# Kernel tuning notes

Measured on AMD Instinct MI355X. Metric: run time of the kernel, lower is better.

Reference implementation:

```python
import jax, jax.numpy as jnp
import numpy as np

B, IN, H, OUT = 4096, 1024, 2048, 1024
EPS = 1e-5  # added to std (not variance), matching the torch module


def _ln(z, a, b):
    # torch.std default is unbiased (ddof=1); eps added to sigma
    mu = jnp.mean(z, axis=1, keepdims=True)
    sigma = jnp.std(z, axis=1, ddof=1, keepdims=True)
    return (z - mu) / (sigma + EPS) * a + b


def setup_inputs() -> dict:
    key = jax.random.key(0)
    ks = iter(jax.random.split(key, 40))
    W = lambda i, o: (jax.random.normal(next(ks), (o, i), jnp.float32) / np.sqrt(i)).astype(jnp.float32)
    bz = lambda o: jnp.zeros((o,), jnp.float32)
    d = {
        "inp": jax.random.normal(next(ks), (B, IN), jnp.float32),
        "h_0": jax.random.normal(next(ks), (B, H), jnp.float32),
        "c_0": jax.random.normal(next(ks), (B, H), jnp.float32),
        # h-side gate linears (H -> H)
        "Wfh": W(H, H), "bfh": bz(H), "Wih": W(H, H), "bih": bz(H),
        "Wch": W(H, H), "bch": bz(H), "Woh": W(H, H), "boh": bz(H),
        # x-side gate linears (IN -> H)
        "Wfx": W(IN, H), "bfx": bz(H), "Wix": W(IN, H), "bix": bz(H),
        "Wcx": W(IN, H), "bcx": bz(H), "Wox": W(IN, H), "box": bz(H),
        # decoder (H -> OUT)
        "Wdec": W(H, OUT), "bdec": bz(OUT),
        # LayerNormalization params (a2 ones, b2 zeros), shape (1, H)
        "ax": jnp.ones((1, H), jnp.float32), "bx": jnp.zeros((1, H), jnp.float32),
        "ah": jnp.ones((1, H), jnp.float32), "bh": jnp.zeros((1, H), jnp.float32),
        "ac": jnp.ones((1, H), jnp.float32), "bc": jnp.zeros((1, H), jnp.float32),
    }
    return d


def reference(inp, h_0, c_0,
              Wfh, bfh, Wih, bih, Wch, bch, Woh, boh,
              Wfx, bfx, Wix, bix, Wcx, bcx, Wox, box,
              Wdec, bdec, ax, bx, ah, bh, ac, bc):
    lin = lambda x, W, b: x @ W.T + b
    gate = lambda wx, bx_, wh, bh_: (_ln(lin(inp, wx, bx_), ax, bx)
                                     + _ln(lin(h_0, wh, bh_), ah, bh))
    f_g = jax.nn.sigmoid(gate(Wfx, bfx, Wfh, bfh))
    i_g = jax.nn.sigmoid(gate(Wix, bix, Wih, bih))
    c_tilda = jnp.tanh(gate(Wcx, bcx, Wch, bch))
    cx = f_g * c_0 + i_g * c_tilda
    o_g = jax.nn.sigmoid(gate(Wox, box, Woh, boh))
    hx = o_g * jnp.tanh(_ln(cx, ac, bc))
    out = lin(hx, Wdec, bdec)  # decoder applied to hidden state (vectorized over batch)
    return (out, hx, cx)
```

## Files before the change

### kernel.cpp

```cpp
#include <hip/hip_runtime.h>

#define NB   4096
#define NIN  1024
#define NH   2048
#define NOUT 1024
#define NH4  8192

typedef short short8 __attribute__((ext_vector_type(8)));
typedef float f32x4 __attribute__((ext_vector_type(4)));
typedef unsigned short ushort8v __attribute__((ext_vector_type(8)));

__device__ __forceinline__ float bf2f(unsigned short u) {
  union { unsigned int i; float f; } c; c.i = ((unsigned int)u) << 16; return c.f;
}
__device__ __forceinline__ unsigned short f2bf(float f) {
  union { float f; unsigned int i; } c; c.f = f;
  unsigned int u = c.i;
  u += 0x7FFFu + ((u >> 16) & 1u);
  return (unsigned short)(u >> 16);
}
__device__ __forceinline__ float sigf(float x) { return 1.0f / (1.0f + __expf(-x)); }
__device__ __forceinline__ float tanh_f(float x) { return 1.0f - 2.0f / (__expf(2.0f * x) + 1.0f); }

#define CNT_INP  ((size_t)NB * NIN)
#define CNT_H0   ((size_t)NB * NH)
#define CNT_WXG  ((size_t)NH * NIN)
#define CNT_WHG  ((size_t)NH * NH)
#define CNT_WD   ((size_t)NOUT * NH)
#define OFF_XB   ((size_t)0)
#define OFF_H0B  (OFF_XB + CNT_INP)
#define OFF_HXB  (OFF_H0B + CNT_H0)
#define OFF_WX   (OFF_HXB + CNT_H0)
#define OFF_WH   (OFF_WX + 4 * CNT_WXG)
#define OFF_WD   (OFF_WH + 4 * CNT_WHG)
#define OFF_ZX   (OFF_WD + CNT_WD)
#define OFF_ZH   (OFF_ZX + (size_t)NB * NH4)
#define CVT_TOTAL (OFF_WD + CNT_WD)

struct CvtArgs { const float* src[11]; };

__global__ __launch_bounds__(256) void cvt_all(CvtArgs a, unsigned short* __restrict__ dstBase) {
  const size_t i = ((size_t)blockIdx.x * 256 + threadIdx.x) * 8;
  if (i >= CVT_TOTAL) return;
  const size_t cnt[11] = {CNT_INP, CNT_H0, CNT_WXG, CNT_WXG, CNT_WXG, CNT_WXG,
                          CNT_WHG, CNT_WHG, CNT_WHG, CNT_WHG, CNT_WD};
  const size_t dst[11] = {OFF_XB, OFF_H0B,
                          OFF_WX, OFF_WX + CNT_WXG, OFF_WX + 2 * CNT_WXG, OFF_WX + 3 * CNT_WXG,
                          OFF_WH, OFF_WH + CNT_WHG, OFF_WH + 2 * CNT_WHG, OFF_WH + 3 * CNT_WHG,
                          OFF_WD};
  size_t base = 0;
#pragma unroll
  for (int s = 0; s < 11; s++) {
    if (i < base + cnt[s]) {
      const size_t off = i - base;
      const float* sp = a.src[s] + off;
      float4 v0 = *(const float4*)(sp);
      float4 v1 = *(const float4*)(sp + 4);
      ushort8v o;
      o[0] = f2bf(v0.x); o[1] = f2bf(v0.y); o[2] = f2bf(v0.z); o[3] = f2bf(v0.w);
      o[4] = f2bf(v1.x); o[5] = f2bf(v1.y); o[6] = f2bf(v1.z); o[7] = f2bf(v1.w);
      *(ushort8v*)(dstBase + dst[s] + off) = o;
      return;
    }
    base += cnt[s];
  }
}

__device__ __forceinline__ void gload16(const void* g, void* l) {
  __builtin_amdgcn_global_load_lds((const __attribute__((address_space(1))) void*)g,
                                   (__attribute__((address_space(3))) void*)l, 16, 0, 0);
}

template<int MF, bool BOUT>
__device__ __forceinline__ void gemm_core(const unsigned short* __restrict__ A,
                                          const unsigned short* __restrict__ Bm,
                                          const float* b0p, const float* b1p,
                                          const float* b2p, const float* b3p,
                                          float* __restrict__ Cf, unsigned short* __restrict__ Cb,
                                          int N, int K) {
  constexpr int TM = MF * 32;
  __shared__ __align__(16) unsigned short As[TM * 32];
  __shared__ __align__(16) unsigned short Bs[128 * 32];
  const int t = threadIdx.x;
  const int w = t >> 6;
  const int lane = t & 63;
  const int m0 = blockIdx.y * TM;
  const int n0 = blockIdx.x * 128;
  const int wm = (w >> 1) * (MF * 16);
  const int wn = (w & 1) * 64;

  f32x4 acc[MF][4];
#pragma unroll
  for (int i = 0; i < MF; i++)
#pragma unroll
    for (int j = 0; j < 4; j++) { f32x4 z = {0.f, 0.f, 0.f, 0.f}; acc[i][j] = z; }

  const int srow = t >> 2;
  const int scb = (t & 3) ^ ((srow >> 1) & 3);
  const unsigned short* Ag = A + (size_t)(m0 + srow) * K + scb * 8;
  const unsigned short* Bg = Bm + (size_t)(n0 + srow) * K + scb * 8;
  const size_t rowStep = (size_t)64 * K;
  unsigned short* AsW0 = As + w * 512;
  unsigned short* AsW1 = (MF == 4) ? (As + 2048 + w * 512) : (As + w * 512);
  unsigned short* BsW0 = Bs + w * 512;
  unsigned short* BsW1 = Bs + 2048 + w * 512;

  const int fr = lane & 15;
  const int fks = (((lane >> 4) ^ ((fr >> 1) & 3)) & 3) * 8;

  for (int k0 = 0; k0 < K; k0 += 32) {
    gload16(Ag + k0, AsW0);
    if (MF == 4) gload16(Ag + rowStep + k0, AsW1);
    gload16(Bg + k0, BsW0);
    gload16(Bg + rowStep + k0, BsW1);
    __syncthreads();

    short8 af[MF], bfr[4];
#pragma unroll
    for (int i = 0; i < MF; i++) af[i] = *(const short8*)&As[(wm + i * 16 + fr) * 32 + fks];
#pragma unroll
    for (int j = 0; j < 4; j++) bfr[j] = *(const short8*)&Bs[(wn + j * 16 + fr) * 32 + fks];
#pragma unroll
    for (int i = 0; i < MF; i++)
#pragma unroll
      for (int j = 0; j < 4; j++)
        acc[i][j] = __builtin_amdgcn_mfma_f32_16x16x32_bf16(af[i], bfr[j], acc[i][j], 0, 0, 0);
    __syncthreads();
  }

  const int cn = lane & 15;
  const int cm = (lane >> 4) * 4;
#pragma unroll
  for (int i = 0; i < MF; i++) {
#pragma unroll
    for (int j = 0; j < 4; j++) {
      const int col = n0 + wn + j * 16 + cn;
      const float* bp = (col < 2048) ? b0p : ((col < 4096) ? b1p : ((col < 6144) ? b2p : b3p));
      const float bv = bp[col & 2047];
      const size_t base = (size_t)(m0 + wm + i * 16 + cm) * N + col;
#pragma unroll
      for (int r = 0; r < 4; r++) {
        const float v = acc[i][j][r] + bv;
        if (BOUT) Cb[base + (size_t)r * N] = f2bf(v);
        else      Cf[base + (size_t)r * N] = v;
      }
    }
  }
}

__global__ __launch_bounds__(256) void gemm_dual(const unsigned short* __restrict__ Xb,
                                                 const unsigned short* __restrict__ Wx,
                                                 const unsigned short* __restrict__ H0b,
                                                 const unsigned short* __restrict__ Wh,
                                                 const float* bx0, const float* bx1,
                                                 const float* bx2, const float* bx3,
                                                 const float* bh0, const float* bh1,
                                                 const float* bh2, const float* bh3,
                                                 unsigned short* __restrict__ Zx,
                                                 unsigned short* __restrict__ Zh) {
  if (blockIdx.z == 0)
    gemm_core<4, true>(Xb, Wx, bx0, bx1, bx2, bx3, nullptr, Zx, NH4, NIN);
  else
    gemm_core<4, true>(H0b, Wh, bh0, bh1, bh2, bh3, nullptr, Zh, NH4, NH);
}

__global__ __launch_bounds__(256) void gemm_dec(const unsigned short* __restrict__ HXb,
                                                const unsigned short* __restrict__ Wd,
                                                const float* __restrict__ bdec,
                                                float* __restrict__ out) {
  gemm_core<2, false>(HXb, Wd, bdec, bdec, bdec, bdec, out, nullptr, NOUT, NH);
}

__global__ __launch_bounds__(256) void ln_gates(const unsigned short* __restrict__ Zx,
                                                const unsigned short* __restrict__ Zh,
                                                const float* __restrict__ c0,
                                                const float* __restrict__ ax, const float* __restrict__ bx,
                                                const float* __restrict__ ah, const float* __restrict__ bh,
                                                const float* __restrict__ ac, const float* __restrict__ bc,
                                                float* __restrict__ out_top,
                                                unsigned short* __restrict__ hx_bf) {
  const int b = blockIdx.x;
  const int t = threadIdx.x;
  const int n = t * 8;
  const int w = t >> 6;
  const int lane = t & 63;
  const float inv_n = 1.0f / 2048.0f, inv_nm1 = 1.0f / 2047.0f;

  short8 zx[4], zh[4];
  const size_t rowoff = (size_t)b * NH4;
#pragma unroll
  for (int g = 0; g < 4; g++) {
    zx[g] = *(const short8*)(Zx + rowoff + g * NH + n);
    zh[g] = *(const short8*)(Zh + rowoff + g * NH + n);
  }

  float s[16];
#pragma unroll
  for (int g = 0; g < 4; g++) {
    float su = 0, sq = 0, su2 = 0, sq2 = 0;
#pragma unroll
    for (int j = 0; j < 8; j++) {
      float v = bf2f((unsigned short)zx[g][j]); su += v; sq += v * v;
      float u = bf2f((unsigned short)zh[g][j]); su2 += u; sq2 += u * u;
    }
    s[g * 4 + 0] = su; s[g * 4 + 1] = sq; s[g * 4 + 2] = su2; s[g * 4 + 3] = sq2;
  }
#pragma unroll
  for (int i = 0; i < 16; i++) {
    float v = s[i];
#pragma unroll
    for (int o = 32; o > 0; o >>= 1) v += __shfl_xor(v, o, 64);
    s[i] = v;
  }
  __shared__ float red[4][16];
  __shared__ float red2[4][2];
  if (lane == 0) {
#pragma unroll
    for (int i = 0; i < 16; i++) red[w][i] = s[i];
  }
  __syncthreads();
#pragma unroll
  for (int i = 0; i < 16; i++) s[i] = red[0][i] + red[1][i] + red[2][i] + red[3][i];

  float mux[4], ivx[4], muh[4], ivh[4];
#pragma unroll
  for (int g = 0; g < 4; g++) {
    mux[g] = s[g * 4 + 0] * inv_n;
    float vx = fmaxf((s[g * 4 + 1] - s[g * 4 + 0] * mux[g]) * inv_nm1, 0.0f);
    ivx[g] = 1.0f / (sqrtf(vx) + 1e-5f);
    muh[g] = s[g * 4 + 2] * inv_n;
    float vh = fmaxf((s[g * 4 + 3] - s[g * 4 + 2] * muh[g]) * inv_nm1, 0.0f);
    ivh[g] = 1.0f / (sqrtf(vh) + 1e-5f);
  }

  float axl[8], bxl[8], ahl[8], bhl[8], c0l[8];
  *(float4*)&axl[0] = *(const float4*)(ax + n); *(float4*)&axl[4] = *(const float4*)(ax + n + 4);
  *(float4*)&bxl[0] = *(const float4*)(bx + n); *(float4*)&bxl[4] = *(const float4*)(bx + n + 4);
  *(float4*)&ahl[0] = *(const float4*)(ah + n); *(float4*)&ahl[4] = *(const float4*)(ah + n + 4);
  *(float4*)&bhl[0] = *(const float4*)(bh + n); *(float4*)&bhl[4] = *(const float4*)(bh + n + 4);
  const float* c0p = c0 + (size_t)b * NH + n;
  *(float4*)&c0l[0] = *(const float4*)(c0p); *(float4*)&c0l[4] = *(const float4*)(c0p + 4);

  float cx[8], og[8];
  float cs = 0, css = 0;
#pragma unroll
  for (int j = 0; j < 8; j++) {
    float pre[4];
#pragma unroll
    for (int g = 0; g < 4; g++) {
      float vx = bf2f((unsigned short)zx[g][j]);
      float vh = bf2f((unsigned short)zh[g][j]);
      pre[g] = ((vx - mux[g]) * ivx[g]) * axl[j] + bxl[j]
             + ((vh - muh[g]) * ivh[g]) * ahl[j] + bhl[j];
    }
    float fg = sigf(pre[0]);
    float ig = sigf(pre[1]);
    float ct = tanh_f(pre[2]);
    og[j] = sigf(pre[3]);
    float c = fg * c0l[j] + ig * ct;
    cx[j] = c; cs += c; css += c * c;
  }
#pragma unroll
  for (int o = 32; o > 0; o >>= 1) { cs += __shfl_xor(cs, o, 64); css += __shfl_xor(css, o, 64); }
  if (lane == 0) { red2[w][0] = cs; red2[w][1] = css; }
  __syncthreads();
  cs = red2[0][0] + red2[1][0] + red2[2][0] + red2[3][0];
  css = red2[0][1] + red2[1][1] + red2[2][1] + red2[3][1];
  const float muc = cs * inv_n;
  const float varc = fmaxf((css - cs * muc) * inv_nm1, 0.0f);
  const float ivc = 1.0f / (sqrtf(varc) + 1e-5f);

  float acl[8], bcl[8];
  *(float4*)&acl[0] = *(const float4*)(ac + n); *(float4*)&acl[4] = *(const float4*)(ac + n + 4);
  *(float4*)&bcl[0] = *(const float4*)(bc + n); *(float4*)&bcl[4] = *(const float4*)(bc + n + 4);

  float hx[8];
#pragma unroll
  for (int j = 0; j < 8; j++)
    hx[j] = og[j] * tanh_f((cx[j] - muc) * ivc * acl[j] + bcl[j]);

  float* hx_out = out_top + (size_t)NB * NOUT + (size_t)b * NH + n;
  float* cx_out = out_top + (size_t)NB * NOUT + (size_t)NB * NH + (size_t)b * NH + n;
  float4 v;
  v.x = hx[0]; v.y = hx[1]; v.z = hx[2]; v.w = hx[3]; *(float4*)(hx_out) = v;
  v.x = hx[4]; v.y = hx[5]; v.z = hx[6]; v.w = hx[7]; *(float4*)(hx_out + 4) = v;
  v.x = cx[0]; v.y = cx[1]; v.z = cx[2]; v.w = cx[3]; *(float4*)(cx_out) = v;
  v.x = cx[4]; v.y = cx[5]; v.z = cx[6]; v.w = cx[7]; *(float4*)(cx_out + 4) = v;
  ushort8v hb;
#pragma unroll
  for (int j = 0; j < 8; j++) hb[j] = f2bf(hx[j]);
  *(ushort8v*)(hx_bf + (size_t)b * NH + n) = hb;
}

extern "C" void kernel_launch(void* const* d_in, const int* in_sizes, int n_in,
                              void* d_out, int out_size, void* d_ws, size_t ws_size,
                              hipStream_t stream) {
  const float* inp = (const float*)d_in[0];
  const float* h0  = (const float*)d_in[1];
  const float* c0  = (const float*)d_in[2];
  const float* bhg[4] = {(const float*)d_in[4], (const float*)d_in[6], (const float*)d_in[8], (const float*)d_in[10]};
  const float* bxg[4] = {(const float*)d_in[12], (const float*)d_in[14], (const float*)d_in[16], (const float*)d_in[18]};
  const float* bdec = (const float*)d_in[20];
  const float* ax = (const float*)d_in[21];
  const float* bx = (const float*)d_in[22];
  const float* ah = (const float*)d_in[23];
  const float* bh = (const float*)d_in[24];
  const float* ac = (const float*)d_in[25];
  const float* bc = (const float*)d_in[26];

  unsigned short* wsb = (unsigned short*)d_ws;
  unsigned short* Xb   = wsb + OFF_XB;
  unsigned short* H0b  = wsb + OFF_H0B;
  unsigned short* HXb  = wsb + OFF_HXB;
  unsigned short* Wx4b = wsb + OFF_WX;
  unsigned short* Wh4b = wsb + OFF_WH;
  unsigned short* Wdb  = wsb + OFF_WD;
  unsigned short* Zx   = wsb + OFF_ZX;
  unsigned short* Zh   = wsb + OFF_ZH;

  CvtArgs ca;
  ca.src[0] = inp; ca.src[1] = h0;
  ca.src[2] = (const float*)d_in[11]; ca.src[3] = (const float*)d_in[13];
  ca.src[4] = (const float*)d_in[15]; ca.src[5] = (const float*)d_in[17];
  ca.src[6] = (const float*)d_in[3];  ca.src[7] = (const float*)d_in[5];
  ca.src[8] = (const float*)d_in[7];  ca.src[9] = (const float*)d_in[9];
  ca.src[10] = (const float*)d_in[19];
  {
    const size_t nthr = CVT_TOTAL / 8;
    cvt_all<<<dim3((unsigned)((nthr + 255) / 256)), dim3(256), 0, stream>>>(ca, wsb);
  }

  gemm_dual<<<dim3(NH4 / 128, NB / 128, 2), 256, 0, stream>>>(
      Xb, Wx4b, H0b, Wh4b,
      bxg[0], bxg[1], bxg[2], bxg[3],
      bhg[0], bhg[1], bhg[2], bhg[3],
      Zx, Zh);

  ln_gates<<<dim3(NB), 256, 0, stream>>>(Zx, Zh, c0, ax, bx, ah, bh, ac, bc, (float*)d_out, HXb);

  gemm_dec<<<dim3(NOUT / 128, NB / 64), 256, 0, stream>>>(HXb, Wdb, bdec, (float*)d_out);
}
```

Measured before the change: 612.6 us.

## Switch GEMM core to 32x32x16 MFMA with BK=64 tiles

Replaces the 16x16x32 bf16 MFMA GEMM core with a 32x32x16 MFMA variant and doubles the K-step per LDS stage from 32 to 64. It uses a new XOR swizzle for LDS staging and new fragment addressing. The block tile shapes stay the same, so LDS per block doubles while barriers per K are halved and the larger MFMA shape gets more reuse per fragment load. The epilogue now follows the 32x32 accumulator row layout.

Measured after the change: 577.1 us. -5.8%, faster.

```diff
diff --git a/kernel.cpp b/kernel.cpp
--- a/kernel.cpp
+++ b/kernel.cpp
@@ -8,6 +8,7 @@
 
 typedef short short8 __attribute__((ext_vector_type(8)));
 typedef float f32x4 __attribute__((ext_vector_type(4)));
+typedef float f32x16 __attribute__((ext_vector_type(16)));
 typedef unsigned short ushort8v __attribute__((ext_vector_type(8)));
 
 __device__ __forceinline__ float bf2f(unsigned short u) {
@@ -71,78 +72,95 @@
                                    (__attribute__((address_space(3))) void*)l, 16, 0, 0);
 }
 
-template<int MF, bool BOUT>
-__device__ __forceinline__ void gemm_core(const unsigned short* __restrict__ A,
-                                          const unsigned short* __restrict__ Bm,
-                                          const float* b0p, const float* b1p,
-                                          const float* b2p, const float* b3p,
-                                          float* __restrict__ Cf, unsigned short* __restrict__ Cb,
-                                          int N, int K) {
-  constexpr int TM = MF * 32;
-  __shared__ __align__(16) unsigned short As[TM * 32];
-  __shared__ __align__(16) unsigned short Bs[128 * 32];
+template<int MT, bool BOUT>
+__device__ __forceinline__ void gemm_core32(const unsigned short* __restrict__ A,
+                                            const unsigned short* __restrict__ Bm,
+                                            const float* b0p, const float* b1p,
+                                            const float* b2p, const float* b3p,
+                                            float* __restrict__ Cf, unsigned short* __restrict__ Cb,
+                                            int N, int K) {
+  constexpr int TM = MT * 64;
+  __shared__ __align__(16) unsigned short As[TM * 64];
+  __shared__ __align__(16) unsigned short Bs[128 * 64];
   const int t = threadIdx.x;
   const int w = t >> 6;
   const int lane = t & 63;
+  const int r31 = lane & 31;
+  const int hi = lane >> 5;
+  const int rloc = lane >> 3;
+  const int slot = lane & 7;
+  const int bblk = slot ^ rloc;
   const int m0 = blockIdx.y * TM;
   const int n0 = blockIdx.x * 128;
-  const int wm = (w >> 1) * (MF * 16);
+  const int wm = (w >> 1) * (MT * 32);
   const int wn = (w & 1) * 64;
 
-  f32x4 acc[MF][4];
-#pragma unroll
-  for (int i = 0; i < MF; i++)
-#pragma unroll
-    for (int j = 0; j < 4; j++) { f32x4 z = {0.f, 0.f, 0.f, 0.f}; acc[i][j] = z; }
-
-  const int srow = t >> 2;
-  const int scb = (t & 3) ^ ((srow >> 1) & 3);
-  const unsigned short* Ag = A + (size_t)(m0 + srow) * K + scb * 8;
-  const unsigned short* Bg = Bm + (size_t)(n0 + srow) * K + scb * 8;
-  const size_t rowStep = (size_t)64 * K;
-  unsigned short* AsW0 = As + w * 512;
-  unsigned short* AsW1 = (MF == 4) ? (As + 2048 + w * 512) : (As + w * 512);
-  unsigned short* BsW0 = Bs + w * 512;
-  unsigned short* BsW1 = Bs + 2048 + w * 512;
-
-  const int fr = lane & 15;
-  const int fks = (((lane >> 4) ^ ((fr >> 1) & 3)) & 3) * 8;
-
-  for (int k0 = 0; k0 < K; k0 += 32) {
-    gload16(Ag + k0, AsW0);
-    if (MF == 4) gload16(Ag + rowStep + k0, AsW1);
-    gload16(Bg + k0, BsW0);
-    gload16(Bg + rowStep + k0, BsW1);
+  f32x16 acc[MT][2];
+#pragma unroll
+  for (int i = 0; i < MT; i++)
+#pragma unroll
+    for (int j = 0; j < 2; j++)
+#pragma unroll
+      for (int r = 0; r < 16; r++) acc[i][j][r] = 0.f;
+
+  const unsigned short* AgP[2 * MT];
+  unsigned short* AsP[2 * MT];
+#pragma unroll
+  for (int q = 0; q < 2 * MT; q++) {
+    const int iss = w + 4 * q;
+    AgP[q] = A + (size_t)(m0 + iss * 8 + rloc) * K + bblk * 8;
+    AsP[q] = As + iss * 512;
+  }
+  const unsigned short* BgP[4];
+  unsigned short* BsP[4];
+#pragma unroll
+  for (int q = 0; q < 4; q++) {
+    const int iss = w + 4 * q;
+    BgP[q] = Bm + (size_t)(n0 + iss * 8 + rloc) * K + bblk * 8;
+    BsP[q] = Bs + iss * 512;
+  }
+
+  const int swz = (r31 & 7);
+
+  for (int k0 = 0; k0 < K; k0 += 64) {
+#pragma unroll
+    for (int q = 0; q < 2 * MT; q++) gload16(AgP[q] + k0, AsP[q]);
+#pragma unroll
+    for (int q = 0; q < 4; q++) gload16(BgP[q] + k0, BsP[q]);
     __syncthreads();
 
-    short8 af[MF], bfr[4];
-#pragma unroll
-    for (int i = 0; i < MF; i++) af[i] = *(const short8*)&As[(wm + i * 16 + fr) * 32 + fks];
-#pragma unroll
-    for (int j = 0; j < 4; j++) bfr[j] = *(const short8*)&Bs[(wn + j * 16 + fr) * 32 + fks];
-#pragma unroll
-    for (int i = 0; i < MF; i++)
-#pragma unroll
-      for (int j = 0; j < 4; j++)
-        acc[i][j] = __builtin_amdgcn_mfma_f32_16x16x32_bf16(af[i], bfr[j], acc[i][j], 0, 0, 0);
+#pragma unroll
+    for (int ks = 0; ks < 4; ks++) {
+      const int phys = ((ks * 2 + hi) ^ swz) * 8;
+      short8 af[MT], bf[2];
+#pragma unroll
+      for (int mt = 0; mt < MT; mt++) af[mt] = *(const short8*)&As[(wm + mt * 32 + r31) * 64 + phys];
+#pragma unroll
+      for (int jt = 0; jt < 2; jt++) bf[jt] = *(const short8*)&Bs[(wn + jt * 32 + r31) * 64 + phys];
+#pragma unroll
+      for (int mt = 0; mt < MT; mt++)
+#pragma unroll
+        for (int jt = 0; jt < 2; jt++)
+          acc[mt][jt] = __builtin_amdgcn_mfma_f32_32x32x16_bf16(af[mt], bf[jt], acc[mt][jt], 0, 0, 0);
+    }
     __syncthreads();
   }
 
-  const int cn = lane & 15;
-  const int cm = (lane >> 4) * 4;
-#pragma unroll
-  for (int i = 0; i < MF; i++) {
-#pragma unroll
-    for (int j = 0; j < 4; j++) {
-      const int col = n0 + wn + j * 16 + cn;
+#pragma unroll
+  for (int mt = 0; mt < MT; mt++) {
+#pragma unroll
+    for (int jt = 0; jt < 2; jt++) {
+      const int col = n0 + wn + jt * 32 + r31;
       const float* bp = (col < 2048) ? b0p : ((col < 4096) ? b1p : ((col < 6144) ? b2p : b3p));
       const float bv = bp[col & 2047];
-      const size_t base = (size_t)(m0 + wm + i * 16 + cm) * N + col;
-#pragma unroll
-      for (int r = 0; r < 4; r++) {
-        const float v = acc[i][j][r] + bv;
-        if (BOUT) Cb[base + (size_t)r * N] = f2bf(v);
-        else      Cf[base + (size_t)r * N] = v;
+      const int rowb = m0 + wm + mt * 32 + hi * 4;
+#pragma unroll
+      for (int reg = 0; reg < 16; reg++) {
+        const int row = rowb + (reg & 3) + 8 * (reg >> 2);
+        const float v = acc[mt][jt][reg] + bv;
+        const size_t idx = (size_t)row * N + col;
+        if (BOUT) Cb[idx] = f2bf(v);
+        else      Cf[idx] = v;
       }
     }
   }
@@ -159,16 +177,16 @@
                                                  unsigned short* __restrict__ Zx,
                                                  unsigned short* __restrict__ Zh) {
   if (blockIdx.z == 0)
-    gemm_core<4, true>(Xb, Wx, bx0, bx1, bx2, bx3, nullptr, Zx, NH4, NIN);
+    gemm_core32<2, true>(Xb, Wx, bx0, bx1, bx2, bx3, nullptr, Zx, NH4, NIN);
   else
-    gemm_core<4, true>(H0b, Wh, bh0, bh1, bh2, bh3, nullptr, Zh, NH4, NH);
+    gemm_core32<2, true>(H0b, Wh, bh0, bh1, bh2, bh3, nullptr, Zh, NH4, NH);
 }
 
 __global__ __launch_bounds__(256) void gemm_dec(const unsigned short* __restrict__ HXb,
                                                 const unsigned short* __restrict__ Wd,
                                                 const float* __restrict__ bdec,
                                                 float* __restrict__ out) {
-  gemm_core<2, false>(HXb, Wd, bdec, bdec, bdec, bdec, out, nullptr, NOUT, NH);
+  gemm_core32<1, false>(HXb, Wd, bdec, bdec, bdec, bdec, out, nullptr, NOUT, NH);
 }
 
 __global__ __launch_bounds__(256) void ln_gates(const unsigned short* __restrict__ Zx,
```
